# Performance work log

Measured on AMD Instinct MI355X. Metric: run time of the kernel, lower is better.

The kernel has to match this reference:

```python
import jax, jax.numpy as jnp
import numpy as np
from jax import lax
import math

LAYERS, STACKS = 10, 3
NL = LAYERS * STACKS          # 30 residual layers
DC, RC, SC, CLASSES, K = 32, 32, 256, 256, 2


def _conv1d(x, w, b, dilation=1, pad_left=0):
    # x: [B, Cin, T], w: [Cout, Cin, Kw]. Left-padding by (Kw-1)*dilation
    # reproduces torch's symmetric pad followed by x[:, :, :T] (causal conv).
    out = lax.conv_general_dilated(
        x, w, window_strides=(1,), padding=[(pad_left, 0)],
        rhs_dilation=(dilation,), dimension_numbers=('NCH', 'OIH', 'NCH'))
    return out + b[None, :, None]


def setup_inputs() -> dict:
    key = jax.random.key(0)
    ks = jax.random.split(key, 13)
    B, T = 4, 32768
    s = jnp.float32(0.05)
    return {
        'y': jax.random.normal(ks[0], (B, CLASSES, T), jnp.float32),
        'W_causal': jax.random.normal(ks[1], (RC, CLASSES, 1)) * s,
        'b_causal': jax.random.normal(ks[2], (RC,)) * s,
        'Wf': jax.random.normal(ks[3], (NL, DC, RC, K)) * s,
        'bf': jax.random.normal(ks[4], (NL, DC)) * s,
        'Wr': jax.random.normal(ks[5], (NL, RC, DC // 2, 1)) * s,
        'br': jax.random.normal(ks[6], (NL, RC)) * s,
        'Ws': jax.random.normal(ks[7], (NL, SC, DC // 2, 1)) * s,
        'bs': jax.random.normal(ks[8], (NL, SC)) * s,
        'W_e1': jax.random.normal(ks[9], (SC, SC, 1)) * s,
        'b_e1': jax.random.normal(ks[10], (SC,)) * s,
        'W_e2': jax.random.normal(ks[11], (CLASSES, SC, 1)) * s,
        'b_e2': jax.random.normal(ks[12], (CLASSES,)) * s,
    }


def reference(y, W_causal, b_causal, Wf, bf, Wr, br, Ws, bs, W_e1, b_e1, W_e2, b_e2):
    # y: [B, 256, T]
    x = _conv1d(y, W_causal, b_causal)                      # [B, RC, T]
    skip = jnp.zeros((y.shape[0], SC, y.shape[2]), y.dtype)
    inv_sqrt2 = jnp.float32(math.sqrt(0.5))
    for i in range(NL):  # fixed 30 structurally distinct layers (dilation varies)
        d = 2 ** (i % LAYERS)
        residual = x
        h = _conv1d(x, Wf[i], bf[i], dilation=d, pad_left=(K - 1) * d)  # [B, DC, T]
        a, b = jnp.split(h, 2, axis=1)                      # each [B, DC//2, T]
        g = jnp.tanh(a) * jax.nn.sigmoid(b)
        skip = skip + _conv1d(g, Ws[i], bs[i])              # [B, SC, T]
        x = (_conv1d(g, Wr[i], br[i]) + residual) * inv_sqrt2
    x = jax.nn.relu(skip)
    x = jax.nn.relu(_conv1d(x, W_e1, b_e1))
    x = _conv1d(x, W_e2, b_e2)                              # [B, CLASSES, T]
    return jnp.transpose(x, (0, 2, 1))                      # [B, T, CLASSES]
```

## Files before the change

kernel.cpp:

```cpp
#include <hip/hip_runtime.h>
#include <hip/hip_bf16.h>


#define B_ 4
#define T_ 32768
#define RC_ 32
#define KH_ 16
#define SC_ 256
#define CLASSES_ 256
#define NL_ 30
#define NT_ 131072L

using f32x4 = __attribute__((ext_vector_type(4))) float;
using s16x8 = __attribute__((ext_vector_type(8))) short;

__device__ inline float fast_rcp(float x) { return __builtin_amdgcn_rcpf(x); }
__device__ inline float fast_sigmoid(float x) { return fast_rcp(1.f + __expf(-x)); }
__device__ inline float fast_tanh(float x) { return 1.f - 2.f * fast_rcp(__expf(2.f * x) + 1.f); }

__device__ inline ushort f2bf(float v) {
    __hip_bfloat16 h = __float2bfloat16(v);
    return __builtin_bit_cast(ushort, h);
}
__device__ inline uint pack2(float a, float b) {
    return (uint)f2bf(a) | ((uint)f2bf(b) << 16);
}
__device__ inline float bflo(uint u) { return __builtin_bit_cast(float, u << 16); }
__device__ inline float bfhi(uint u) { return __builtin_bit_cast(float, u & 0xffff0000u); }
__device__ inline s16x8 mfma_in(uint4 u) { return __builtin_bit_cast(s16x8, u); }

__global__ __launch_bounds__(256) void prep_w_kernel(
    const float* __restrict__ Wc, const float* __restrict__ Wf,
    const float* __restrict__ Wr, const float* __restrict__ Ws,
    const float* __restrict__ We1, const float* __restrict__ We2,
    ushort* __restrict__ wcp, ushort* __restrict__ wfp, ushort* __restrict__ wrp,
    ushort* __restrict__ wst, ushort* __restrict__ we1b, ushort* __restrict__ we2b)
{
    int j = blockIdx.x * 256 + threadIdx.x;
    if (j < 24576) {
        int m = j / 768, k = j % 768;
        float v = Wc[m * 256 + (k & 255)];
        if (k < 512) wcp[j] = f2bf(v);
        else {
            float hi = __bfloat162float(__float2bfloat16(v));
            wcp[j] = f2bf(v - hi);
        }
    } else if (j < 86016) {
        int e = j - 24576;
        int i = e >> 11; int r = e & 2047;
        int tap = r >> 10, c = (r >> 5) & 31, ci = r & 31;
        wfp[e] = f2bf(Wf[((size_t)(i * 32 + c) * 32 + ci) * 2 + tap]);
    } else if (j < 116736) {
        int e = j - 86016;
        int i = e >> 10; int c = (e >> 5) & 31; int k = e & 31;
        wrp[e] = (k < 16) ? f2bf(Wr[(size_t)(i * 32 + c) * 16 + k]) : (ushort)0;
    } else if (j < 239616) {
        int e = j - 116736;
        int s = e / 480, k = e % 480;
        int i = k >> 4, ci = k & 15;
        wst[e] = f2bf(Ws[(size_t)(i * 256 + s) * 16 + ci]);
    } else if (j < 305152) {
        int e = j - 239616; we1b[e] = f2bf(We1[e]);
    } else if (j < 370688) {
        int e = j - 305152; we2b[e] = f2bf(We2[e]);
    }
}

__global__ void bsum_kernel(const float* __restrict__ bs, float* __restrict__ bsSum) {
    int s = threadIdx.x;
    float v = 0.f;
    #pragma unroll
    for (int i = 0; i < NL_; ++i) v += bs[i * SC_ + s];
    bsSum[s] = v;
}

__global__ __launch_bounds__(256) void prep_y_kernel(
    const float* __restrict__ y, ushort* __restrict__ y_t)
{
    __shared__ float lds[32][65];
    int tid = threadIdx.x;
    int b = blockIdx.x >> 9;
    long t0 = (long)(blockIdx.x & 511) * 64;
    for (int cc = 0; cc < 8; ++cc) {
        int c = cc * 32 + (tid >> 3);
        int tp = (tid & 7) * 8;
        const float* src = y + ((size_t)b * 256 + c) * T_ + t0 + tp;
        float4 v0 = *(const float4*)src;
        float4 v1 = *(const float4*)(src + 4);
        lds[tid >> 3][tp + 0] = v0.x; lds[tid >> 3][tp + 1] = v0.y;
        lds[tid >> 3][tp + 2] = v0.z; lds[tid >> 3][tp + 3] = v0.w;
        lds[tid >> 3][tp + 4] = v1.x; lds[tid >> 3][tp + 5] = v1.y;
        lds[tid >> 3][tp + 6] = v1.z; lds[tid >> 3][tp + 7] = v1.w;
        __syncthreads();
        int t = tid & 63, cp = tid >> 6;
        float v[8];
        #pragma unroll
        for (int jj = 0; jj < 8; ++jj) v[jj] = lds[cp * 8 + jj][t];
        uint hi[4], lo[4];
        #pragma unroll
        for (int jj = 0; jj < 4; ++jj) {
            float a = v[2 * jj], bv = v[2 * jj + 1];
            float ah = __bfloat162float(__float2bfloat16(a));
            float bh = __bfloat162float(__float2bfloat16(bv));
            hi[jj] = pack2(a, bv);
            lo[jj] = pack2(a - ah, bv - bh);
        }
        ushort* dst = y_t + ((size_t)b * T_ + t0 + t) * 512 + cc * 32 + cp * 8;
        *(uint4*)dst = make_uint4(hi[0], hi[1], hi[2], hi[3]);
        *(uint4*)(dst + 256) = make_uint4(lo[0], lo[1], lo[2], lo[3]);
        __syncthreads();
    }
}

__global__ __launch_bounds__(256) void init_gemm_kernel(
    const ushort* __restrict__ wcp, const ushort* __restrict__ y_t,
    const float* __restrict__ bc, ushort* __restrict__ x0)
{
    __shared__ ushort sa[2][32 * 40];
    __shared__ ushort sb[2][256 * 40];
    int tid = threadIdx.x;
    int wid = tid >> 6, lane = tid & 63, q = lane >> 4, ln = lane & 15;
    long n0 = (long)blockIdx.x * 256;

    uint4 ar0, ar1, br0, br1, br2, br3;
    auto load_tile = [&](int kc) {
        int k0 = kc * 32;
        int koff = (k0 < 512) ? k0 : k0 - 512;
        if (tid < 64) {
            int m = tid >> 1, h = tid & 1;
            const uint4* s = (const uint4*)(wcp + m * 768 + k0 + h * 16);
            ar0 = s[0]; ar1 = s[1];
        }
        const uint4* sB = (const uint4*)(y_t + (n0 + tid) * 512 + koff);
        br0 = sB[0]; br1 = sB[1]; br2 = sB[2]; br3 = sB[3];
    };
    auto store_tile = [&](int buf) {
        if (tid < 64) {
            int m = tid >> 1, h = tid & 1;
            *(uint4*)&sa[buf][m * 40 + h * 16] = ar0;
            *(uint4*)&sa[buf][m * 40 + h * 16 + 8] = ar1;
        }
        *(uint4*)&sb[buf][tid * 40 + 0]  = br0;
        *(uint4*)&sb[buf][tid * 40 + 8]  = br1;
        *(uint4*)&sb[buf][tid * 40 + 16] = br2;
        *(uint4*)&sb[buf][tid * 40 + 24] = br3;
    };

    f32x4 acc[2][4];
    #pragma unroll
    for (int mi = 0; mi < 2; ++mi) {
        f32x4 bv = *(const f32x4*)&bc[mi * 16 + 4 * q];
        #pragma unroll
        for (int ni = 0; ni < 4; ++ni) acc[mi][ni] = bv;
    }
    load_tile(0);
    for (int kc = 0; kc < 24; ++kc) {
        int buf = kc & 1;
        store_tile(buf);
        __syncthreads();
        if (kc + 1 < 24) load_tile(kc + 1);
        s16x8 af[2];
        #pragma unroll
        for (int mi = 0; mi < 2; ++mi)
            af[mi] = mfma_in(*(const uint4*)&sa[buf][(mi * 16 + ln) * 40 + q * 8]);
        #pragma unroll
        for (int ni = 0; ni < 4; ++ni) {
            s16x8 bfr = mfma_in(*(const uint4*)&sb[buf][(wid * 64 + ni * 16 + ln) * 40 + q * 8]);
            #pragma unroll
            for (int mi = 0; mi < 2; ++mi)
                acc[mi][ni] = __builtin_amdgcn_mfma_f32_16x16x32_bf16(af[mi], bfr, acc[mi][ni], 0, 0, 0);
        }
        __syncthreads();
    }
    #pragma unroll
    for (int mi = 0; mi < 2; ++mi) {
        int ch = mi * 16 + 4 * q;
        #pragma unroll
        for (int ni = 0; ni < 4; ++ni) {
            long t = n0 + wid * 64 + ni * 16 + ln;
            f32x4 v = acc[mi][ni];
            uint2 pk; pk.x = pack2(v[0], v[1]); pk.y = pack2(v[2], v[3]);
            *(uint2*)&x0[t * 32 + ch] = pk;
        }
    }
}

__global__ __launch_bounds__(256) void layer_mfma_kernel(
    const ushort* __restrict__ xb_in, ushort* __restrict__ xb_out,
    ushort* __restrict__ g_out,
    const ushort* __restrict__ wfp, const ushort* __restrict__ wrp,
    const float* __restrict__ bfp, const float* __restrict__ brp, int d)
{
    int tid = threadIdx.x;
    int wid = tid >> 6, lane = tid & 63, q = lane >> 4, ln = lane & 15;
    long tw = (long)blockIdx.x * 128 + wid * 32;

    s16x8 wfA[2][2], wrA[2];
    #pragma unroll
    for (int mb = 0; mb < 2; ++mb) {
        #pragma unroll
        for (int tap = 0; tap < 2; ++tap)
            wfA[mb][tap] = mfma_in(*(const uint4*)&wfp[(tap * 32 + mb * 16 + ln) * 32 + q * 8]);
        wrA[mb] = mfma_in(*(const uint4*)&wrp[(mb * 16 + ln) * 32 + q * 8]);
    }
    f32x4 bfv0 = *(const f32x4*)&bfp[4 * q];
    f32x4 bfv1 = *(const f32x4*)&bfp[16 + 4 * q];
    f32x4 brv0 = *(const f32x4*)&brp[4 * q];
    f32x4 brv1 = *(const f32x4*)&brp[16 + 4 * q];
    const float inv_s2 = 0.70710678118654752f;

    #pragma unroll
    for (int nb = 0; nb < 2; ++nb) {
        long t = tw + nb * 16 + ln;
        bool vok = ((int)(t & (T_ - 1)) >= d);
        long r0 = vok ? (t - d) : t;
        uint4 u0 = *(const uint4*)&xb_in[r0 * 32 + 8 * q];
        if (!vok) u0 = make_uint4(0, 0, 0, 0);
        uint4 u1 = *(const uint4*)&xb_in[t * 32 + 8 * q];
        s16x8 b0 = mfma_in(u0), b1 = mfma_in(u1);

        f32x4 h0 = {}, h1 = {};
        h0 = __builtin_amdgcn_mfma_f32_16x16x32_bf16(wfA[0][0], b0, h0, 0, 0, 0);
        h0 = __builtin_amdgcn_mfma_f32_16x16x32_bf16(wfA[0][1], b1, h0, 0, 0, 0);
        h1 = __builtin_amdgcn_mfma_f32_16x16x32_bf16(wfA[1][0], b0, h1, 0, 0, 0);
        h1 = __builtin_amdgcn_mfma_f32_16x16x32_bf16(wfA[1][1], b1, h1, 0, 0, 0);

        float g[4];
        #pragma unroll
        for (int r = 0; r < 4; ++r)
            g[r] = fast_tanh(h0[r] + bfv0[r]) * fast_sigmoid(h1[r] + bfv1[r]);
        uint p01 = pack2(g[0], g[1]), p23 = pack2(g[2], g[3]);
        uint2 gst; gst.x = p01; gst.y = p23;
        *(uint2*)&g_out[t * 16 + 4 * q] = gst;

        int sA = q * 32 + ln;
        uint f0 = (uint)__shfl((int)p01, sA);
        uint f1 = (uint)__shfl((int)p23, sA);
        uint f2 = (uint)__shfl((int)p01, sA + 16);
        uint f3 = (uint)__shfl((int)p23, sA + 16);
        s16x8 gb = mfma_in(make_uint4(f0, f1, f2, f3));

        f32x4 rr0 = {}, rr1 = {};
        rr0 = __builtin_amdgcn_mfma_f32_16x16x32_bf16(wrA[0], gb, rr0, 0, 0, 0);
        rr1 = __builtin_amdgcn_mfma_f32_16x16x32_bf16(wrA[1], gb, rr1, 0, 0, 0);

        uint2 xr0 = *(const uint2*)&xb_in[t * 32 + 4 * q];
        uint2 xr1 = *(const uint2*)&xb_in[t * 32 + 16 + 4 * q];
        float o00 = (rr0[0] + brv0[0] + bflo(xr0.x)) * inv_s2;
        float o01 = (rr0[1] + brv0[1] + bfhi(xr0.x)) * inv_s2;
        float o02 = (rr0[2] + brv0[2] + bflo(xr0.y)) * inv_s2;
        float o03 = (rr0[3] + brv0[3] + bfhi(xr0.y)) * inv_s2;
        float o10 = (rr1[0] + brv1[0] + bflo(xr1.x)) * inv_s2;
        float o11 = (rr1[1] + brv1[1] + bfhi(xr1.x)) * inv_s2;
        float o12 = (rr1[2] + brv1[2] + bflo(xr1.y)) * inv_s2;
        float o13 = (rr1[3] + brv1[3] + bfhi(xr1.y)) * inv_s2;
        uint2 xp0; xp0.x = pack2(o00, o01); xp0.y = pack2(o02, o03);
        uint2 xp1; xp1.x = pack2(o10, o11); xp1.y = pack2(o12, o13);
        *(uint2*)&xb_out[t * 32 + 4 * q] = xp0;
        *(uint2*)&xb_out[t * 32 + 16 + 4 * q] = xp1;
    }
}

__global__ __launch_bounds__(256) void tail_kernel(
    const ushort* __restrict__ g_all, const float* __restrict__ bsSum,
    const ushort* __restrict__ wst, const ushort* __restrict__ we1b,
    const ushort* __restrict__ we2b, const float* __restrict__ be1,
    const float* __restrict__ be2, float* __restrict__ out)
{
    __shared__ ushort sa[256 * 40];
    __shared__ ushort pq[8 * 64 * 40];
    ushort* sb = pq;
    int tid = threadIdx.x;
    int wid = tid >> 6, lane = tid & 63, q = lane >> 4, ln = lane & 15;
    long n0 = (long)blockIdx.x * 64;
    int wrow = wid * 64;

    f32x4 acc[4][4];
    #pragma unroll
    for (int mi = 0; mi < 4; ++mi) {
        f32x4 bv = *(const f32x4*)&bsSum[wrow + mi * 16 + 4 * q];
        #pragma unroll
        for (int ni = 0; ni < 4; ++ni) acc[mi][ni] = bv;
    }
    for (int kc = 0; kc < 15; ++kc) {
        __syncthreads();
        {
            const uint4* s = (const uint4*)(wst + (size_t)tid * 480 + kc * 32);
            uint4 a0 = s[0], a1 = s[1], a2 = s[2], a3 = s[3];
            *(uint4*)&sa[tid * 40 + 0]  = a0;
            *(uint4*)&sa[tid * 40 + 8]  = a1;
            *(uint4*)&sa[tid * 40 + 16] = a2;
            *(uint4*)&sa[tid * 40 + 24] = a3;
        }
        {
            int n = tid & 63, ip = (tid >> 6) & 1, half = tid >> 7;
            uint4 b0 = *(const uint4*)(g_all +
                ((size_t)(2 * kc + ip) * NT_ + n0 + n) * 16 + half * 8);
            *(uint4*)&sb[n * 40 + ip * 16 + half * 8] = b0;
        }
        __syncthreads();
        s16x8 af[4];
        #pragma unroll
        for (int mi = 0; mi < 4; ++mi)
            af[mi] = mfma_in(*(const uint4*)&sa[(wrow + mi * 16 + ln) * 40 + q * 8]);
        #pragma unroll
        for (int ni = 0; ni < 4; ++ni) {
            s16x8 bfr = mfma_in(*(const uint4*)&sb[(ni * 16 + ln) * 40 + q * 8]);
            #pragma unroll
            for (int mi = 0; mi < 4; ++mi)
                acc[mi][ni] = __builtin_amdgcn_mfma_f32_16x16x32_bf16(af[mi], bfr, acc[mi][ni], 0, 0, 0);
        }
    }
    __syncthreads();
    #pragma unroll
    for (int mi = 0; mi < 4; ++mi) {
        int ch = wrow + mi * 16 + 4 * q;
        int base = (ch >> 5) * 2560, c5 = ch & 31;
        #pragma unroll
        for (int ni = 0; ni < 4; ++ni) {
            f32x4 v = acc[mi][ni];
            int ta = base + (ni * 16 + ln) * 40 + c5;
            *(uint*)&pq[ta]     = pack2(fmaxf(v[0], 0.f), fmaxf(v[1], 0.f));
            *(uint*)&pq[ta + 2] = pack2(fmaxf(v[2], 0.f), fmaxf(v[3], 0.f));
        }
    }
    #pragma unroll
    for (int mi = 0; mi < 4; ++mi) {
        f32x4 bv = *(const f32x4*)&be1[wrow + mi * 16 + 4 * q];
        #pragma unroll
        for (int ni = 0; ni < 4; ++ni) acc[mi][ni] = bv;
    }
    for (int kc = 0; kc < 8; ++kc) {
        __syncthreads();
        {
            const uint4* s = (const uint4*)(we1b + (size_t)tid * 256 + kc * 32);
            uint4 a0 = s[0], a1 = s[1], a2 = s[2], a3 = s[3];
            *(uint4*)&sa[tid * 40 + 0]  = a0;
            *(uint4*)&sa[tid * 40 + 8]  = a1;
            *(uint4*)&sa[tid * 40 + 16] = a2;
            *(uint4*)&sa[tid * 40 + 24] = a3;
        }
        __syncthreads();
        s16x8 af[4];
        #pragma unroll
        for (int mi = 0; mi < 4; ++mi)
            af[mi] = mfma_in(*(const uint4*)&sa[(wrow + mi * 16 + ln) * 40 + q * 8]);
        #pragma unroll
        for (int ni = 0; ni < 4; ++ni) {
            s16x8 bfr = mfma_in(*(const uint4*)&pq[kc * 2560 + (ni * 16 + ln) * 40 + q * 8]);
            #pragma unroll
            for (int mi = 0; mi < 4; ++mi)
                acc[mi][ni] = __builtin_amdgcn_mfma_f32_16x16x32_bf16(af[mi], bfr, acc[mi][ni], 0, 0, 0);
        }
    }
    __syncthreads();
    #pragma unroll
    for (int mi = 0; mi < 4; ++mi) {
        int ch = wrow + mi * 16 + 4 * q;
        int base = (ch >> 5) * 2560, c5 = ch & 31;
        #pragma unroll
        for (int ni = 0; ni < 4; ++ni) {
            f32x4 v = acc[mi][ni];
            int ta = base + (ni * 16 + ln) * 40 + c5;
            *(uint*)&pq[ta]     = pack2(fmaxf(v[0], 0.f), fmaxf(v[1], 0.f));
            *(uint*)&pq[ta + 2] = pack2(fmaxf(v[2], 0.f), fmaxf(v[3], 0.f));
        }
    }
    #pragma unroll
    for (int mi = 0; mi < 4; ++mi) {
        f32x4 bv = *(const f32x4*)&be2[wrow + mi * 16 + 4 * q];
        #pragma unroll
        for (int ni = 0; ni < 4; ++ni) acc[mi][ni] = bv;
    }
    for (int kc = 0; kc < 8; ++kc) {
        __syncthreads();
        {
            const uint4* s = (const uint4*)(we2b + (size_t)tid * 256 + kc * 32);
            uint4 a0 = s[0], a1 = s[1], a2 = s[2], a3 = s[3];
            *(uint4*)&sa[tid * 40 + 0]  = a0;
            *(uint4*)&sa[tid * 40 + 8]  = a1;
            *(uint4*)&sa[tid * 40 + 16] = a2;
            *(uint4*)&sa[tid * 40 + 24] = a3;
        }
        __syncthreads();
        s16x8 af[4];
        #pragma unroll
        for (int mi = 0; mi < 4; ++mi)
            af[mi] = mfma_in(*(const uint4*)&sa[(wrow + mi * 16 + ln) * 40 + q * 8]);
        #pragma unroll
        for (int ni = 0; ni < 4; ++ni) {
            s16x8 bfr = mfma_in(*(const uint4*)&pq[kc * 2560 + (ni * 16 + ln) * 40 + q * 8]);
            #pragma unroll
            for (int mi = 0; mi < 4; ++mi)
                acc[mi][ni] = __builtin_amdgcn_mfma_f32_16x16x32_bf16(af[mi], bfr, acc[mi][ni], 0, 0, 0);
        }
    }
    #pragma unroll
    for (int mi = 0; mi < 4; ++mi) {
        int ch = wrow + mi * 16 + 4 * q;
        #pragma unroll
        for (int ni = 0; ni < 4; ++ni) {
            long t = n0 + ni * 16 + ln;
            *(f32x4*)&out[t * 256 + ch] = acc[mi][ni];
        }
    }
}

__device__ inline float load_g(const float* p) { return *p; }
__device__ inline float load_g(const __hip_bfloat16* p) { return __bfloat162float(*p); }
__device__ inline void store_g(float* p, float v) { *p = v; }
__device__ inline void store_g(__hip_bfloat16* p, float v) { *p = __float2bfloat16(v); }

__global__ __launch_bounds__(256) void init_conv_kernel(
    const float* __restrict__ y, const float* __restrict__ Wc,
    const float* __restrict__ bc, float* __restrict__ x0)
{
    int gid = blockIdx.x * 256 + threadIdx.x;
    int b = gid >> 15;
    int t = gid & (T_ - 1);
    float acc[RC_];
    #pragma unroll
    for (int c = 0; c < RC_; ++c) acc[c] = bc[c];
    const float* yb = y + (size_t)b * CLASSES_ * T_ + t;
    for (int cb = 0; cb < CLASSES_; cb += 32) {
        float yv[32];
        #pragma unroll
        for (int j = 0; j < 32; ++j) yv[j] = yb[(size_t)(cb + j) * T_];
        #pragma unroll
        for (int c = 0; c < RC_; ++c)
            #pragma unroll
            for (int j = 0; j < 32; ++j)
                acc[c] = fmaf(Wc[c * CLASSES_ + cb + j], yv[j], acc[c]);
    }
    float* xo = x0 + (size_t)b * RC_ * T_ + t;
    #pragma unroll
    for (int c = 0; c < RC_; ++c) xo[(size_t)c * T_] = acc[c];
}

template <typename G>
__global__ __launch_bounds__(256) void layer_kernel(
    const float* __restrict__ x_in, float* __restrict__ x_out, G* __restrict__ g_out,
    const float* __restrict__ wf, const float* __restrict__ bfp,
    const float* __restrict__ wr, const float* __restrict__ brp, int d)
{
    int gid = blockIdx.x * 256 + threadIdx.x;
    int b = gid >> 15;
    int t = gid & (T_ - 1);
    const float* xbase = x_in + (size_t)b * RC_ * T_ + t;
    float xm[RC_], xd[RC_];
    #pragma unroll
    for (int ci = 0; ci < RC_; ++ci) xm[ci] = xbase[(size_t)ci * T_];
    #pragma unroll
    for (int ci = 0; ci < RC_; ++ci)
        xd[ci] = (t >= d) ? xbase[(size_t)ci * T_ - d] : 0.f;
    float a_[KH_];
    #pragma unroll
    for (int c = 0; c < KH_; ++c) {
        float s = bfp[c];
        #pragma unroll
        for (int ci = 0; ci < RC_; ++ci) {
            s = fmaf(wf[(c * RC_ + ci) * 2 + 0], xd[ci], s);
            s = fmaf(wf[(c * RC_ + ci) * 2 + 1], xm[ci], s);
        }
        a_[c] = s;
    }
    float g[KH_];
    #pragma unroll
    for (int c = 0; c < KH_; ++c) {
        float s = bfp[KH_ + c];
        #pragma unroll
        for (int ci = 0; ci < RC_; ++ci) {
            s = fmaf(wf[((KH_ + c) * RC_ + ci) * 2 + 0], xd[ci], s);
            s = fmaf(wf[((KH_ + c) * RC_ + ci) * 2 + 1], xm[ci], s);
        }
        g[c] = fast_tanh(a_[c]) * fast_sigmoid(s);
    }
    G* gb = g_out + (size_t)b * KH_ * T_ + t;
    #pragma unroll
    for (int c = 0; c < KH_; ++c) store_g(gb + (size_t)c * T_, g[c]);
    float* xo = x_out + (size_t)b * RC_ * T_ + t;
    #pragma unroll
    for (int c = 0; c < RC_; ++c) {
        float s = brp[c];
        #pragma unroll
        for (int ci = 0; ci < KH_; ++ci) s = fmaf(wr[c * KH_ + ci], g[ci], s);
        xo[(size_t)c * T_] = (s + xm[c]) * 0.70710678118654752f;
    }
}

template <typename G>
__global__ __launch_bounds__(256) void final_kernel(
    const G* __restrict__ g_all, const float* __restrict__ bsSum,
    const float* __restrict__ Ws, const float* __restrict__ We1,
    const float* __restrict__ be1, const float* __restrict__ We2,
    const float* __restrict__ be2, float* __restrict__ out)
{
    __shared__ float smem[14336];
    float* plds = smem;
    float* qlds = smem + 5120;
    float* glds = smem;
    float* wlds = smem + 10240;
    int tid = threadIdx.x;
    int bt = blockIdx.x;
    int b = bt >> 11;
    int t0 = (bt & 2047) << 4;
    int c4 = tid & 63;
    int th = tid >> 6;
    for (int e = tid; e < 480 * 16; e += 256) {
        int row = e >> 4, col = e & 15;
        int i = row >> 4, ci = row & 15;
        glds[e] = load_g(g_all + ((size_t)(i * B_ + b) * KH_ + ci) * T_ + t0 + col);
    }
    __syncthreads();
    float acc[4][4];
    #pragma unroll
    for (int j = 0; j < 4; ++j) {
        float bv = bsSum[c4 + 64 * j];
        #pragma unroll
        for (int tt = 0; tt < 4; ++tt) acc[j][tt] = bv;
    }
    for (int i = 0; i < NL_; ++i) {
        const float4* wsrc = (const float4*)(Ws + ((size_t)i * 256 + tid) * 16);
        float4 w0 = wsrc[0], w1 = wsrc[1], w2 = wsrc[2], w3 = wsrc[3];
        __syncthreads();
        wlds[0*256+tid]=w0.x; wlds[1*256+tid]=w0.y; wlds[2*256+tid]=w0.z; wlds[3*256+tid]=w0.w;
        wlds[4*256+tid]=w1.x; wlds[5*256+tid]=w1.y; wlds[6*256+tid]=w1.z; wlds[7*256+tid]=w1.w;
        wlds[8*256+tid]=w2.x; wlds[9*256+tid]=w2.y; wlds[10*256+tid]=w2.z; wlds[11*256+tid]=w2.w;
        wlds[12*256+tid]=w3.x; wlds[13*256+tid]=w3.y; wlds[14*256+tid]=w3.z; wlds[15*256+tid]=w3.w;
        __syncthreads();
        #pragma unroll
        for (int ci = 0; ci < 16; ++ci) {
            const float4 gv = *(const float4*)&glds[(i * 16 + ci) * 16 + th * 4];
            float wv[4];
            #pragma unroll
            for (int j = 0; j < 4; ++j) wv[j] = wlds[ci * 256 + c4 + 64 * j];
            #pragma unroll
            for (int j = 0; j < 4; ++j) {
                acc[j][0] = fmaf(wv[j], gv.x, acc[j][0]);
                acc[j][1] = fmaf(wv[j], gv.y, acc[j][1]);
                acc[j][2] = fmaf(wv[j], gv.z, acc[j][2]);
                acc[j][3] = fmaf(wv[j], gv.w, acc[j][3]);
            }
        }
    }
    __syncthreads();
    #pragma unroll
    for (int j = 0; j < 4; ++j)
        #pragma unroll
        for (int tt = 0; tt < 4; ++tt)
            plds[(c4 + 64 * j) * 20 + th * 4 + tt] = fmaxf(acc[j][tt], 0.f);
    #pragma unroll
    for (int j = 0; j < 4; ++j) {
        float bv = be1[c4 + 64 * j];
        #pragma unroll
        for (int tt = 0; tt < 4; ++tt) acc[j][tt] = bv;
    }
    for (int kc = 0; kc < 16; ++kc) {
        const float4* wsrc = (const float4*)(We1 + (size_t)tid * 256 + kc * 16);
        float4 w0 = wsrc[0], w1 = wsrc[1], w2 = wsrc[2], w3 = wsrc[3];
        __syncthreads();
        wlds[0*256+tid]=w0.x; wlds[1*256+tid]=w0.y; wlds[2*256+tid]=w0.z; wlds[3*256+tid]=w0.w;
        wlds[4*256+tid]=w1.x; wlds[5*256+tid]=w1.y; wlds[6*256+tid]=w1.z; wlds[7*256+tid]=w1.w;
        wlds[8*256+tid]=w2.x; wlds[9*256+tid]=w2.y; wlds[10*256+tid]=w2.z; wlds[11*256+tid]=w2.w;
        wlds[12*256+tid]=w3.x; wlds[13*256+tid]=w3.y; wlds[14*256+tid]=w3.z; wlds[15*256+tid]=w3.w;
        __syncthreads();
        #pragma unroll
        for (int kk = 0; kk < 16; ++kk) {
            const float4 pv = *(const float4*)&plds[(kc * 16 + kk) * 20 + th * 4];
            float wv[4];
            #pragma unroll
            for (int j = 0; j < 4; ++j) wv[j] = wlds[kk * 256 + c4 + 64 * j];
            #pragma unroll
            for (int j = 0; j < 4; ++j) {
                acc[j][0] = fmaf(wv[j], pv.x, acc[j][0]);
                acc[j][1] = fmaf(wv[j], pv.y, acc[j][1]);
                acc[j][2] = fmaf(wv[j], pv.z, acc[j][2]);
                acc[j][3] = fmaf(wv[j], pv.w, acc[j][3]);
            }
        }
    }
    __syncthreads();
    #pragma unroll
    for (int j = 0; j < 4; ++j)
        #pragma unroll
        for (int tt = 0; tt < 4; ++tt)
            qlds[(c4 + 64 * j) * 20 + th * 4 + tt] = fmaxf(acc[j][tt], 0.f);
    #pragma unroll
    for (int j = 0; j < 4; ++j) {
        float bv = be2[c4 + 64 * j];
        #pragma unroll
        for (int tt = 0; tt < 4; ++tt) acc[j][tt] = bv;
    }
    for (int kc = 0; kc < 16; ++kc) {
        const float4* wsrc = (const float4*)(We2 + (size_t)tid * 256 + kc * 16);
        float4 w0 = wsrc[0], w1 = wsrc[1], w2 = wsrc[2], w3 = wsrc[3];
        __syncthreads();
        wlds[0*256+tid]=w0.x; wlds[1*256+tid]=w0.y; wlds[2*256+tid]=w0.z; wlds[3*256+tid]=w0.w;
        wlds[4*256+tid]=w1.x; wlds[5*256+tid]=w1.y; wlds[6*256+tid]=w1.z; wlds[7*256+tid]=w1.w;
        wlds[8*256+tid]=w2.x; wlds[9*256+tid]=w2.y; wlds[10*256+tid]=w2.z; wlds[11*256+tid]=w2.w;
        wlds[12*256+tid]=w3.x; wlds[13*256+tid]=w3.y; wlds[14*256+tid]=w3.z; wlds[15*256+tid]=w3.w;
        __syncthreads();
        #pragma unroll
        for (int kk = 0; kk < 16; ++kk) {
            const float4 qv = *(const float4*)&qlds[(kc * 16 + kk) * 20 + th * 4];
            float wv[4];
            #pragma unroll
            for (int j = 0; j < 4; ++j) wv[j] = wlds[kk * 256 + c4 + 64 * j];
            #pragma unroll
            for (int j = 0; j < 4; ++j) {
                acc[j][0] = fmaf(wv[j], qv.x, acc[j][0]);
                acc[j][1] = fmaf(wv[j], qv.y, acc[j][1]);
                acc[j][2] = fmaf(wv[j], qv.z, acc[j][2]);
                acc[j][3] = fmaf(wv[j], qv.w, acc[j][3]);
            }
        }
    }
    #pragma unroll
    for (int tt = 0; tt < 4; ++tt) {
        size_t orow = ((size_t)b * T_ + t0 + th * 4 + tt) * 256;
        #pragma unroll
        for (int j = 0; j < 4; ++j)
            out[orow + c4 + 64 * j] = acc[j][tt];
    }
}

template <typename G>
static void run_pipeline_old(const float* y, const float* Wc, const float* bc,
                             const float* Wf, const float* bf, const float* Wr,
                             const float* br, const float* Ws, const float* bs,
                             const float* We1, const float* be1, const float* We2,
                             const float* be2, float* out, char* ws, hipStream_t stream)
{
    size_t xbytes = (size_t)B_ * RC_ * T_ * sizeof(float);
    float* xa = (float*)ws;
    float* xb = (float*)(ws + xbytes);
    G* g_all = (G*)(ws + 2 * xbytes);
    size_t gbytes = (size_t)NL_ * B_ * KH_ * T_ * sizeof(G);
    float* bsSum = (float*)(ws + 2 * xbytes + gbytes);
    bsum_kernel<<<1, 256, 0, stream>>>(bs, bsSum);
    init_conv_kernel<<<512, 256, 0, stream>>>(y, Wc, bc, xa);
    float* xin = xa; float* xout = xb;
    for (int i = 0; i < NL_; ++i) {
        int d = 1 << (i % 10);
        layer_kernel<G><<<512, 256, 0, stream>>>(
            xin, xout, g_all + (size_t)i * B_ * KH_ * T_,
            Wf + (size_t)i * RC_ * RC_ * 2, bf + (size_t)i * RC_,
            Wr + (size_t)i * RC_ * KH_, br + (size_t)i * RC_, d);
        float* tmp = xin; xin = xout; xout = tmp;
    }
    final_kernel<G><<<B_ * (T_ / 16), 256, 0, stream>>>(
        g_all, bsSum, Ws, We1, be1, We2, be2, out);
}

extern "C" void kernel_launch(void* const* d_in, const int* in_sizes, int n_in,
                              void* d_out, int out_size, void* d_ws, size_t ws_size,
                              hipStream_t stream)
{
    (void)in_sizes; (void)n_in; (void)out_size;
    const float* y   = (const float*)d_in[0];
    const float* Wc  = (const float*)d_in[1];
    const float* bc  = (const float*)d_in[2];
    const float* Wf  = (const float*)d_in[3];
    const float* bf  = (const float*)d_in[4];
    const float* Wr  = (const float*)d_in[5];
    const float* br  = (const float*)d_in[6];
    const float* Ws  = (const float*)d_in[7];
    const float* bs  = (const float*)d_in[8];
    const float* We1 = (const float*)d_in[9];
    const float* be1 = (const float*)d_in[10];
    const float* We2 = (const float*)d_in[11];
    const float* be2 = (const float*)d_in[12];
    float* out = (float*)d_out;
    char* ws = (char*)d_ws;

    size_t o = 0;
    auto alloc = [&](size_t bytes) { size_t r = o; o += (bytes + 1023) & ~(size_t)1023; return r; };
    size_t o_reg = alloc(NT_ * 512 * 2);
    size_t o_xa  = alloc(NT_ * 32 * 2);
    size_t o_xb  = alloc(NT_ * 32 * 2);
    size_t o_wcp = alloc(24576 * 2);
    size_t o_wfp = alloc(61440 * 2);
    size_t o_wrp = alloc(30720 * 2);
    size_t o_wst = alloc(122880 * 2);
    size_t o_we1 = alloc(65536 * 2);
    size_t o_we2 = alloc(65536 * 2);
    size_t o_bss = alloc(1024);
    size_t need_new = o;

    if (ws_size >= need_new) {
        ushort* y_t  = (ushort*)(ws + o_reg);
        ushort* g    = (ushort*)(ws + o_reg);
        ushort* xba  = (ushort*)(ws + o_xa);
        ushort* xbb  = (ushort*)(ws + o_xb);
        ushort* wcp  = (ushort*)(ws + o_wcp);
        ushort* wfp  = (ushort*)(ws + o_wfp);
        ushort* wrp  = (ushort*)(ws + o_wrp);
        ushort* wst  = (ushort*)(ws + o_wst);
        ushort* we1b = (ushort*)(ws + o_we1);
        ushort* we2b = (ushort*)(ws + o_we2);
        float*  bsSum= (float*)(ws + o_bss);

        prep_w_kernel<<<1448, 256, 0, stream>>>(Wc, Wf, Wr, Ws, We1, We2,
                                                wcp, wfp, wrp, wst, we1b, we2b);
        bsum_kernel<<<1, 256, 0, stream>>>(bs, bsSum);
        prep_y_kernel<<<2048, 256, 0, stream>>>(y, y_t);
        init_gemm_kernel<<<512, 256, 0, stream>>>(wcp, y_t, bc, xba);

        ushort* xbin = xba; ushort* xbout = xbb;
        for (int i = 0; i < NL_; ++i) {
            int d = 1 << (i % 10);
            layer_mfma_kernel<<<1024, 256, 0, stream>>>(
                xbin, xbout, g + (size_t)i * NT_ * 16,
                wfp + (size_t)i * 2048, wrp + (size_t)i * 1024,
                bf + i * 32, br + i * 32, d);
            ushort* tmp = xbin; xbin = xbout; xbout = tmp;
        }

        tail_kernel<<<2048, 256, 0, stream>>>(g, bsSum, wst, we1b, we2b,
                                              be1, be2, out);
        return;
    }

    size_t xbytes = (size_t)B_ * RC_ * T_ * sizeof(float);
    size_t need_f32 = 2 * xbytes + (size_t)NL_ * B_ * KH_ * T_ * 4 + 1024;
    if (ws_size >= need_f32)
        run_pipeline_old<float>(y, Wc, bc, Wf, bf, Wr, br, Ws, bs, We1, be1, We2, be2, out, ws, stream);
    else
        run_pipeline_old<__hip_bfloat16>(y, Wc, bc, Wf, bf, Wr, br, Ws, bs, We1, be1, We2, be2, out, ws, stream);
}
```

Before: 727.3 us.

## Pre-swizzle tail weights into MFMA fragment order and double-buffer skip staging

Weights for the skip, end1 and end2 projections are rearranged in the prep kernel into per-lane MFMA fragment order. The tail kernel can then load A fragments straight from global memory instead of staging them through LDS with two barriers per k-step. The gated-activation staging now uses a double-buffered LDS tile with register prefetch of the next chunk, and the intermediate LDS buffer uses a fragment-contiguous layout. LDS use drops and launch bounds allow 4 blocks per CU, at the cost of every wave re-reading weight fragments from L2 or global memory.

```diff
diff --git a/kernel.cpp b/kernel.cpp
--- a/kernel.cpp
+++ b/kernel.cpp
@@ -34,7 +34,7 @@
     const float* __restrict__ Wr, const float* __restrict__ Ws,
     const float* __restrict__ We1, const float* __restrict__ We2,
     ushort* __restrict__ wcp, ushort* __restrict__ wfp, ushort* __restrict__ wrp,
-    ushort* __restrict__ wst, ushort* __restrict__ we1b, ushort* __restrict__ we2b)
+    ushort* __restrict__ wsF, ushort* __restrict__ we1F, ushort* __restrict__ we2F)
 {
     int j = blockIdx.x * 256 + threadIdx.x;
     if (j < 24576) {
@@ -56,13 +56,23 @@
         wrp[e] = (k < 16) ? f2bf(Wr[(size_t)(i * 32 + c) * 16 + k]) : (ushort)0;
     } else if (j < 239616) {
         int e = j - 116736;
-        int s = e / 480, k = e % 480;
+        int jj = e & 7, lane = (e >> 3) & 63, mrow = (e >> 9) & 15, kc = e >> 13;
+        int m = mrow * 16 + (lane & 15);
+        int k = kc * 32 + (lane >> 4) * 8 + jj;
         int i = k >> 4, ci = k & 15;
-        wst[e] = f2bf(Ws[(size_t)(i * 256 + s) * 16 + ci]);
+        wsF[e] = f2bf(Ws[((size_t)i * 256 + m) * 16 + ci]);
     } else if (j < 305152) {
-        int e = j - 239616; we1b[e] = f2bf(We1[e]);
+        int e = j - 239616;
+        int jj = e & 7, lane = (e >> 3) & 63, mrow = (e >> 9) & 15, kc = e >> 13;
+        int m = mrow * 16 + (lane & 15);
+        int k = kc * 32 + (lane >> 4) * 8 + jj;
+        we1F[e] = f2bf(We1[m * 256 + k]);
     } else if (j < 370688) {
-        int e = j - 305152; we2b[e] = f2bf(We2[e]);
+        int e = j - 305152;
+        int jj = e & 7, lane = (e >> 3) & 63, mrow = (e >> 9) & 15, kc = e >> 13;
+        int m = mrow * 16 + (lane & 15);
+        int k = kc * 32 + (lane >> 4) * 8 + jj;
+        we2F[e] = f2bf(We2[m * 256 + k]);
     }
 }
 
@@ -261,20 +271,22 @@
     }
 }
 
-__global__ __launch_bounds__(256) void tail_kernel(
+__global__ __launch_bounds__(256, 4) void tail_kernel(
     const ushort* __restrict__ g_all, const float* __restrict__ bsSum,
-    const ushort* __restrict__ wst, const ushort* __restrict__ we1b,
-    const ushort* __restrict__ we2b, const float* __restrict__ be1,
+    const ushort* __restrict__ wsF, const ushort* __restrict__ we1F,
+    const ushort* __restrict__ we2F, const float* __restrict__ be1,
     const float* __restrict__ be2, float* __restrict__ out)
 {
-    __shared__ ushort sa[256 * 40];
-    __shared__ ushort pq[8 * 64 * 40];
-    ushort* sb = pq;
+    __shared__ ushort stg[2][2048];
+    __shared__ ushort pq[16384];
     int tid = threadIdx.x;
     int wid = tid >> 6, lane = tid & 63, q = lane >> 4, ln = lane & 15;
     long n0 = (long)blockIdx.x * 64;
     int wrow = wid * 64;
 
+    int sn = tid & 63, sip = (tid >> 6) & 1, shalf = tid >> 7;
+    int sdst = ((sn >> 4) * 64 + (sip * 2 + shalf) * 16 + (sn & 15)) * 8;
+
     f32x4 acc[4][4];
     #pragma unroll
     for (int mi = 0; mi < 4; ++mi) {
@@ -282,48 +294,45 @@
         #pragma unroll
         for (int ni = 0; ni < 4; ++ni) acc[mi][ni] = bv;
     }
+
+    uint4 ld = *(const uint4*)(g_all + ((size_t)sip * NT_ + n0 + sn) * 16 + shalf * 8);
+    *(uint4*)&stg[0][sdst] = ld;
     for (int kc = 0; kc < 15; ++kc) {
         __syncthreads();
-        {
-            const uint4* s = (const uint4*)(wst + (size_t)tid * 480 + kc * 32);
-            uint4 a0 = s[0], a1 = s[1], a2 = s[2], a3 = s[3];
-            *(uint4*)&sa[tid * 40 + 0]  = a0;
-            *(uint4*)&sa[tid * 40 + 8]  = a1;
-            *(uint4*)&sa[tid * 40 + 16] = a2;
-            *(uint4*)&sa[tid * 40 + 24] = a3;
-        }
-        {
-            int n = tid & 63, ip = (tid >> 6) & 1, half = tid >> 7;
-            uint4 b0 = *(const uint4*)(g_all +
-                ((size_t)(2 * kc + ip) * NT_ + n0 + n) * 16 + half * 8);
-            *(uint4*)&sb[n * 40 + ip * 16 + half * 8] = b0;
-        }
-        __syncthreads();
-        s16x8 af[4];
+        if (kc < 14)
+            ld = *(const uint4*)(g_all +
+                ((size_t)(2 * (kc + 1) + sip) * NT_ + n0 + sn) * 16 + shalf * 8);
+        s16x8 af[4], bfr[4];
         #pragma unroll
         for (int mi = 0; mi < 4; ++mi)
-            af[mi] = mfma_in(*(const uint4*)&sa[(wrow + mi * 16 + ln) * 40 + q * 8]);
-        #pragma unroll
-        for (int ni = 0; ni < 4; ++ni) {
-            s16x8 bfr = mfma_in(*(const uint4*)&sb[(ni * 16 + ln) * 40 + q * 8]);
+            af[mi] = mfma_in(*(const uint4*)(wsF +
+                (((size_t)kc * 16 + wid * 4 + mi) * 64 + lane) * 8));
+        #pragma unroll
+        for (int ni = 0; ni < 4; ++ni)
+            bfr[ni] = mfma_in(*(const uint4*)&stg[kc & 1][(ni * 64 + lane) * 8]);
+        #pragma unroll
+        for (int ni = 0; ni < 4; ++ni)
             #pragma unroll
             for (int mi = 0; mi < 4; ++mi)
-                acc[mi][ni] = __builtin_amdgcn_mfma_f32_16x16x32_bf16(af[mi], bfr, acc[mi][ni], 0, 0, 0);
-        }
-    }
-    __syncthreads();
+                acc[mi][ni] = __builtin_amdgcn_mfma_f32_16x16x32_bf16(
+                    af[mi], bfr[ni], acc[mi][ni], 0, 0, 0);
+        if (kc < 14) *(uint4*)&stg[(kc + 1) & 1][sdst] = ld;
+    }
     #pragma unroll
     for (int mi = 0; mi < 4; ++mi) {
         int ch = wrow + mi * 16 + 4 * q;
-        int base = (ch >> 5) * 2560, c5 = ch & 31;
+        int dbase = ((ch >> 5) * 4) * 512 + (((ch & 31) >> 3) * 16 + ln) * 8 + (ch & 7);
         #pragma unroll
         for (int ni = 0; ni < 4; ++ni) {
             f32x4 v = acc[mi][ni];
-            int ta = base + (ni * 16 + ln) * 40 + c5;
-            *(uint*)&pq[ta]     = pack2(fmaxf(v[0], 0.f), fmaxf(v[1], 0.f));
-            *(uint*)&pq[ta + 2] = pack2(fmaxf(v[2], 0.f), fmaxf(v[3], 0.f));
-        }
-    }
+            uint2 pk;
+            pk.x = pack2(fmaxf(v[0], 0.f), fmaxf(v[1], 0.f));
+            pk.y = pack2(fmaxf(v[2], 0.f), fmaxf(v[3], 0.f));
+            *(uint2*)&pq[dbase + ni * 512] = pk;
+        }
+    }
+    __syncthreads();
+
     #pragma unroll
     for (int mi = 0; mi < 4; ++mi) {
         f32x4 bv = *(const f32x4*)&be1[wrow + mi * 16 + 4 * q];
@@ -331,41 +340,37 @@
         for (int ni = 0; ni < 4; ++ni) acc[mi][ni] = bv;
     }
     for (int kc = 0; kc < 8; ++kc) {
-        __syncthreads();
-        {
-            const uint4* s = (const uint4*)(we1b + (size_t)tid * 256 + kc * 32);
-            uint4 a0 = s[0], a1 = s[1], a2 = s[2], a3 = s[3];
-            *(uint4*)&sa[tid * 40 + 0]  = a0;
-            *(uint4*)&sa[tid * 40 + 8]  = a1;
-            *(uint4*)&sa[tid * 40 + 16] = a2;
-            *(uint4*)&sa[tid * 40 + 24] = a3;
-        }
-        __syncthreads();
-        s16x8 af[4];
+        s16x8 af[4], bfr[4];
         #pragma unroll
         for (int mi = 0; mi < 4; ++mi)
-            af[mi] = mfma_in(*(const uint4*)&sa[(wrow + mi * 16 + ln) * 40 + q * 8]);
-        #pragma unroll
-        for (int ni = 0; ni < 4; ++ni) {
-            s16x8 bfr = mfma_in(*(const uint4*)&pq[kc * 2560 + (ni * 16 + ln) * 40 + q * 8]);
+            af[mi] = mfma_in(*(const uint4*)(we1F +
+                (((size_t)kc * 16 + wid * 4 + mi) * 64 + lane) * 8));
+        #pragma unroll
+        for (int ni = 0; ni < 4; ++ni)
+            bfr[ni] = mfma_in(*(const uint4*)&pq[(kc * 4 + ni) * 512 + lane * 8]);
+        #pragma unroll
+        for (int ni = 0; ni < 4; ++ni)
             #pragma unroll
             for (int mi = 0; mi < 4; ++mi)
-                acc[mi][ni] = __builtin_amdgcn_mfma_f32_16x16x32_bf16(af[mi], bfr, acc[mi][ni], 0, 0, 0);
-        }
+                acc[mi][ni] = __builtin_amdgcn_mfma_f32_16x16x32_bf16(
+                    af[mi], bfr[ni], acc[mi][ni], 0, 0, 0);
     }
     __syncthreads();
     #pragma unroll
     for (int mi = 0; mi < 4; ++mi) {
         int ch = wrow + mi * 16 + 4 * q;
-        int base = (ch >> 5) * 2560, c5 = ch & 31;
+        int dbase = ((ch >> 5) * 4) * 512 + (((ch & 31) >> 3) * 16 + ln) * 8 + (ch & 7);
         #pragma unroll
         for (int ni = 0; ni < 4; ++ni) {
             f32x4 v = acc[mi][ni];
-            int ta = base + (ni * 16 + ln) * 40 + c5;
-            *(uint*)&pq[ta]     = pack2(fmaxf(v[0], 0.f), fmaxf(v[1], 0.f));
-            *(uint*)&pq[ta + 2] = pack2(fmaxf(v[2], 0.f), fmaxf(v[3], 0.f));
-        }
-    }
+            uint2 pk;
+            pk.x = pack2(fmaxf(v[0], 0.f), fmaxf(v[1], 0.f));
+            pk.y = pack2(fmaxf(v[2], 0.f), fmaxf(v[3], 0.f));
+            *(uint2*)&pq[dbase + ni * 512] = pk;
+        }
+    }
+    __syncthreads();
+
     #pragma unroll
     for (int mi = 0; mi < 4; ++mi) {
         f32x4 bv = *(const f32x4*)&be2[wrow + mi * 16 + 4 * q];
@@ -373,27 +378,20 @@
         for (int ni = 0; ni < 4; ++ni) acc[mi][ni] = bv;
     }
     for (int kc = 0; kc < 8; ++kc) {
-        __syncthreads();
-        {
-            const uint4* s = (const uint4*)(we2b + (size_t)tid * 256 + kc * 32);
-            uint4 a0 = s[0], a1 = s[1], a2 = s[2], a3 = s[3];
-            *(uint4*)&sa[tid * 40 + 0]  = a0;
-            *(uint4*)&sa[tid * 40 + 8]  = a1;
-            *(uint4*)&sa[tid * 40 + 16] = a2;
-            *(uint4*)&sa[tid * 40 + 24] = a3;
-        }
-        __syncthreads();
-        s16x8 af[4];
+        s16x8 af[4], bfr[4];
         #pragma unroll
         for (int mi = 0; mi < 4; ++mi)
-            af[mi] = mfma_in(*(const uint4*)&sa[(wrow + mi * 16 + ln) * 40 + q * 8]);
-        #pragma unroll
-        for (int ni = 0; ni < 4; ++ni) {
-            s16x8 bfr = mfma_in(*(const uint4*)&pq[kc * 2560 + (ni * 16 + ln) * 40 + q * 8]);
+            af[mi] = mfma_in(*(const uint4*)(we2F +
+                (((size_t)kc * 16 + wid * 4 + mi) * 64 + lane) * 8));
+        #pragma unroll
+        for (int ni = 0; ni < 4; ++ni)
+            bfr[ni] = mfma_in(*(const uint4*)&pq[(kc * 4 + ni) * 512 + lane * 8]);
+        #pragma unroll
+        for (int ni = 0; ni < 4; ++ni)
             #pragma unroll
             for (int mi = 0; mi < 4; ++mi)
-                acc[mi][ni] = __builtin_amdgcn_mfma_f32_16x16x32_bf16(af[mi], bfr, acc[mi][ni], 0, 0, 0);
-        }
+                acc[mi][ni] = __builtin_amdgcn_mfma_f32_16x16x32_bf16(
+                    af[mi], bfr[ni], acc[mi][ni], 0, 0, 0);
     }
     #pragma unroll
     for (int mi = 0; mi < 4; ++mi) {
@@ -695,13 +693,13 @@
         ushort* wcp  = (ushort*)(ws + o_wcp);
         ushort* wfp  = (ushort*)(ws + o_wfp);
         ushort* wrp  = (ushort*)(ws + o_wrp);
-        ushort* wst  = (ushort*)(ws + o_wst);
-        ushort* we1b = (ushort*)(ws + o_we1);
-        ushort* we2b = (ushort*)(ws + o_we2);
+        ushort* wsF  = (ushort*)(ws + o_wst);
+        ushort* we1F = (ushort*)(ws + o_we1);
+        ushort* we2F = (ushort*)(ws + o_we2);
         float*  bsSum= (float*)(ws + o_bss);
 
         prep_w_kernel<<<1448, 256, 0, stream>>>(Wc, Wf, Wr, Ws, We1, We2,
-                                                wcp, wfp, wrp, wst, we1b, we2b);
+                                                wcp, wfp, wrp, wsF, we1F, we2F);
         bsum_kernel<<<1, 256, 0, stream>>>(bs, bsSum);
         prep_y_kernel<<<2048, 256, 0, stream>>>(y, y_t);
         init_gemm_kernel<<<512, 256, 0, stream>>>(wcp, y_t, bc, xba);
@@ -716,7 +714,7 @@
             ushort* tmp = xbin; xbin = xbout; xbout = tmp;
         }
 
-        tail_kernel<<<2048, 256, 0, stream>>>(g, bsSum, wst, we1b, we2b,
+        tail_kernel<<<2048, 256, 0, stream>>>(g, bsSum, wsF, we1F, we2F,
                                               be1, be2, out);
         return;
     }
```

New measurement: 690.6 us. 1.05x faster.
